# Performance work log

Hardware: AMD Instinct MI355X
Metric: run time of the kernel (lower is better)

Reference implementation:

```python
import jax, jax.numpy as jnp
import numpy as np

K_EFF = 8           # top-k factors selected per token (init k, < num_factors)
TEMPERATURE = 1.0   # forward() default


def setup_inputs() -> dict:
    key = jax.random.key(0)
    k1, k2 = jax.random.split(key)
    N, M = 131072, 512
    logits = jax.random.normal(k1, (N, M), dtype=jnp.float32)
    beta_qb = jax.random.normal(k2, (M,), dtype=jnp.float32)
    return {"logits": logits, "beta_qb": beta_qb}


def reference(logits, beta_qb):
    """Quantile-balanced sparse gating forward (eval path).

    Top-k selection on debiased logits (logits - beta_qb); probabilities are a
    softmax over the selected RAW logits, scattered back to a dense [N, M] map.
    """
    N, M = logits.shape
    # debiased scores only steer the hard top-k selection
    scores_adj = logits - beta_qb[None, :]                 # [N, M]
    _, topk_idx = jax.lax.top_k(scores_adj, K_EFF)         # [N, k]
    # gather raw logits at selected factors, softmax over the k slots
    selected = jnp.take_along_axis(logits, topk_idx, axis=-1)   # [N, k]
    selected_probs = jax.nn.softmax(selected / TEMPERATURE, axis=-1)
    # scatter sparse probabilities back into dense [N, M]
    rows = jnp.arange(N)[:, None]                          # [N, 1]
    probs = jnp.zeros_like(logits).at[rows, topk_idx].set(selected_probs)
    return probs
```

## Files before the change

### kernel.cpp

```cpp
#include <hip/hip_runtime.h>


constexpr int M_DIM = 512;

template<int CTRL, int RMASK>
__device__ __forceinline__ unsigned wmax_step(unsigned v) {
    int y = __builtin_amdgcn_update_dpp((int)v, (int)v, CTRL, RMASK, 0xF, false);
    unsigned u = (unsigned)y;
    return u > v ? u : v;
}

__device__ __forceinline__ unsigned wave_max_u32(unsigned v) {
    v = wmax_step<0x111, 0xF>(v);
    v = wmax_step<0x112, 0xF>(v);
    v = wmax_step<0x114, 0xF>(v);
    v = wmax_step<0x118, 0xF>(v);
    v = wmax_step<0x142, 0xA>(v);
    v = wmax_step<0x143, 0xC>(v);
    return (unsigned)__builtin_amdgcn_readlane((int)v, 63);
}

template<int S>
__device__ __forceinline__ void round_step(unsigned key[8], const float raw[8],
                                           unsigned M[8], unsigned win,
                                           float& rawt, int lane, bool rereduce) {
    unsigned long long mm = __ballot(key[S] == win);
    int wl = (int)__builtin_ctzll(mm);
    rawt = __int_as_float(__builtin_amdgcn_readlane(__float_as_int(raw[S]), wl));
    if (lane == wl) key[S] = 0u;
    if (rereduce) M[S] = wave_max_u32(key[S]);
}

__global__ __launch_bounds__(256, 8)
void qb_gating_kernel(const float* __restrict__ logits,
                      const float* __restrict__ beta,
                      float* __restrict__ out,
                      int nrows)
{
    const int lane   = threadIdx.x & 63;
    const int gwave  = (int)((blockIdx.x * blockDim.x + threadIdx.x) >> 6);
    const int nwaves = (int)((gridDim.x * blockDim.x) >> 6);

    const int base0 = 4 * lane;
    const int base1 = 256 + 4 * lane;

    const float4 b0 = *(const float4*)(beta + base0);
    const float4 b1 = *(const float4*)(beta + base1);
    const float bb[8] = {b0.x, b0.y, b0.z, b0.w, b1.x, b1.y, b1.z, b1.w};

    for (int row = gwave; row < nrows; row += nwaves) {
        const float* rp = logits + (size_t)row * M_DIM;
        const float4 r0 = *(const float4*)(rp + base0);
        const float4 r1 = *(const float4*)(rp + base1);
        float raw[8] = {r0.x, r0.y, r0.z, r0.w, r1.x, r1.y, r1.z, r1.w};

        unsigned key[8];
#pragma unroll
        for (int s = 0; s < 8; ++s) {
            const float a = raw[s] - bb[s];
            const int u = __float_as_int(a);
            key[s] = (unsigned)(u ^ ((u >> 31) | 0x80000000));
        }

        unsigned M[8];
#pragma unroll
        for (int s = 0; s < 8; ++s) M[s] = wave_max_u32(key[s]);

        float sraw[8];
#pragma unroll
        for (int t = 0; t < 8; ++t) {
            unsigned best = M[0]; int ss = 0;
#pragma unroll
            for (int s = 1; s < 8; ++s) {
                if (M[s] > best) { best = M[s]; ss = s; }
            }
#define ROUND_CASE(S) case S: round_step<S>(key, raw, M, best, sraw[t], lane, t < 7); break;
            switch (ss) {
                ROUND_CASE(0) ROUND_CASE(1) ROUND_CASE(2) ROUND_CASE(3)
                ROUND_CASE(4) ROUND_CASE(5) ROUND_CASE(6) ROUND_CASE(7)
            }
#undef ROUND_CASE
        }

        float m = sraw[0];
#pragma unroll
        for (int t = 1; t < 8; ++t) m = fmaxf(m, sraw[t]);
        float sum = 0.f;
#pragma unroll
        for (int t = 0; t < 8; ++t) sum += __expf(sraw[t] - m);
        const float inv = __builtin_amdgcn_rcpf(sum);

        float o[8];
#pragma unroll
        for (int s = 0; s < 8; ++s)
            o[s] = (key[s] == 0u) ? __expf(raw[s] - m) * inv : 0.f;

        float* op = out + (size_t)row * M_DIM;
        *(float4*)(op + base0) = make_float4(o[0], o[1], o[2], o[3]);
        *(float4*)(op + base1) = make_float4(o[4], o[5], o[6], o[7]);
    }
}

extern "C" void kernel_launch(void* const* d_in, const int* in_sizes, int n_in,
                              void* d_out, int out_size, void* d_ws, size_t ws_size,
                              hipStream_t stream)
{
    const float* logits = (const float*)d_in[0];
    const float* beta   = (const float*)d_in[1];
    float*       out    = (float*)d_out;

    const int nrows = in_sizes[0] / M_DIM;

    qb_gating_kernel<<<4096, 256, 0, stream>>>(logits, beta, out, nrows);
}
```

Before: 449.9 us.

## Replace iterative argmax top-k with ballot-based binary search on threshold

Instead of eight rounds of wave max reductions to extract top-k, the kernel binary-searches the 32-bit sortable key space for a threshold where exactly 8 elements are at or above it, counting with ballots and popcounts. Ties at the boundary are broken by lane prefix counts. The softmax now uses exp of raw logits without max subtraction and a DPP wave sum. This risks overflow for large logits and can take up to 32 search iterations of 8 ballots each per row.

```diff
diff --git a/kernel.cpp b/kernel.cpp
--- a/kernel.cpp
+++ b/kernel.cpp
@@ -4,31 +4,19 @@
 constexpr int M_DIM = 512;
 
 template<int CTRL, int RMASK>
-__device__ __forceinline__ unsigned wmax_step(unsigned v) {
-    int y = __builtin_amdgcn_update_dpp((int)v, (int)v, CTRL, RMASK, 0xF, false);
-    unsigned u = (unsigned)y;
-    return u > v ? u : v;
+__device__ __forceinline__ float wsum_step(float v) {
+    int y = __builtin_amdgcn_update_dpp(0, __float_as_int(v), CTRL, RMASK, 0xF, true);
+    return v + __int_as_float(y);
 }
 
-__device__ __forceinline__ unsigned wave_max_u32(unsigned v) {
-    v = wmax_step<0x111, 0xF>(v);
-    v = wmax_step<0x112, 0xF>(v);
-    v = wmax_step<0x114, 0xF>(v);
-    v = wmax_step<0x118, 0xF>(v);
-    v = wmax_step<0x142, 0xA>(v);
-    v = wmax_step<0x143, 0xC>(v);
-    return (unsigned)__builtin_amdgcn_readlane((int)v, 63);
-}
-
-template<int S>
-__device__ __forceinline__ void round_step(unsigned key[8], const float raw[8],
-                                           unsigned M[8], unsigned win,
-                                           float& rawt, int lane, bool rereduce) {
-    unsigned long long mm = __ballot(key[S] == win);
-    int wl = (int)__builtin_ctzll(mm);
-    rawt = __int_as_float(__builtin_amdgcn_readlane(__float_as_int(raw[S]), wl));
-    if (lane == wl) key[S] = 0u;
-    if (rereduce) M[S] = wave_max_u32(key[S]);
+__device__ __forceinline__ float wave_sum_f32(float v) {
+    v = wsum_step<0x111, 0xF>(v);
+    v = wsum_step<0x112, 0xF>(v);
+    v = wsum_step<0x114, 0xF>(v);
+    v = wsum_step<0x118, 0xF>(v);
+    v = wsum_step<0x142, 0xA>(v);
+    v = wsum_step<0x143, 0xC>(v);
+    return __int_as_float(__builtin_amdgcn_readlane(__float_as_int(v), 63));
 }
 
 __global__ __launch_bounds__(256, 8)
@@ -52,52 +40,69 @@
         const float* rp = logits + (size_t)row * M_DIM;
         const float4 r0 = *(const float4*)(rp + base0);
         const float4 r1 = *(const float4*)(rp + base1);
-        float raw[8] = {r0.x, r0.y, r0.z, r0.w, r1.x, r1.y, r1.z, r1.w};
+        const float raw[8] = {r0.x, r0.y, r0.z, r0.w, r1.x, r1.y, r1.z, r1.w};
 
         unsigned key[8];
 #pragma unroll
         for (int s = 0; s < 8; ++s) {
-            const float a = raw[s] - bb[s];
-            const int u = __float_as_int(a);
+            const int u = __float_as_int(raw[s] - bb[s]);
             key[s] = (unsigned)(u ^ ((u >> 31) | 0x80000000));
         }
 
-        unsigned M[8];
+        unsigned lo = 0u, hi = 0xFFFFFFFFu, T = 0u;
+        bool found = false;
+        while (hi - lo > 1u) {
+            const unsigned mid = lo + ((hi - lo) >> 1);
+            int c = 0;
 #pragma unroll
-        for (int s = 0; s < 8; ++s) M[s] = wave_max_u32(key[s]);
-
-        float sraw[8];
-#pragma unroll
-        for (int t = 0; t < 8; ++t) {
-            unsigned best = M[0]; int ss = 0;
-#pragma unroll
-            for (int s = 1; s < 8; ++s) {
-                if (M[s] > best) { best = M[s]; ss = s; }
+            for (int s = 0; s < 8; ++s)
+                c += __popcll(__ballot(key[s] >= mid));
+            if (c >= 8) {
+                lo = mid;
+                if (c == 8) { T = mid; found = true; break; }
+            } else {
+                hi = mid;
             }
-#define ROUND_CASE(S) case S: round_step<S>(key, raw, M, best, sraw[t], lane, t < 7); break;
-            switch (ss) {
-                ROUND_CASE(0) ROUND_CASE(1) ROUND_CASE(2) ROUND_CASE(3)
-                ROUND_CASE(4) ROUND_CASE(5) ROUND_CASE(6) ROUND_CASE(7)
-            }
-#undef ROUND_CASE
         }
 
-        float m = sraw[0];
+        bool sel[8];
+        if (found) {
 #pragma unroll
-        for (int t = 1; t < 8; ++t) m = fmaxf(m, sraw[t]);
-        float sum = 0.f;
+            for (int s = 0; s < 8; ++s) sel[s] = key[s] >= T;
+        } else {
+            int need = 8;
 #pragma unroll
-        for (int t = 0; t < 8; ++t) sum += __expf(sraw[t] - m);
-        const float inv = __builtin_amdgcn_rcpf(sum);
+            for (int s = 0; s < 8; ++s) {
+                sel[s] = key[s] > lo;
+                need -= __popcll(__ballot(sel[s]));
+            }
+#pragma unroll
+            for (int s = 0; s < 8; ++s) {
+                const unsigned long long m = __ballot(key[s] == lo);
+                int take = (int)__popcll(m);
+                take = take < need ? take : need;
+                const int pfx = (int)__builtin_amdgcn_mbcnt_hi(
+                    (unsigned)(m >> 32),
+                    __builtin_amdgcn_mbcnt_lo((unsigned)m, 0u));
+                if ((key[s] == lo) && (pfx < take)) sel[s] = true;
+                need -= take;
+            }
+        }
 
-        float o[8];
+        float e[8];
+        float psum = 0.f;
 #pragma unroll
-        for (int s = 0; s < 8; ++s)
-            o[s] = (key[s] == 0u) ? __expf(raw[s] - m) * inv : 0.f;
+        for (int s = 0; s < 8; ++s) {
+            const float ex = __expf(raw[s]);
+            e[s] = sel[s] ? ex : 0.f;
+            psum += e[s];
+        }
+        const float tot = wave_sum_f32(psum);
+        const float inv = __builtin_amdgcn_rcpf(tot);
 
         float* op = out + (size_t)row * M_DIM;
-        *(float4*)(op + base0) = make_float4(o[0], o[1], o[2], o[3]);
-        *(float4*)(op + base1) = make_float4(o[4], o[5], o[6], o[7]);
+        *(float4*)(op + base0) = make_float4(e[0]*inv, e[1]*inv, e[2]*inv, e[3]*inv);
+        *(float4*)(op + base1) = make_float4(e[4]*inv, e[5]*inv, e[6]*inv, e[7]*inv);
     }
 }
 
```

New measurement: 443.7 us. About the same (-1.4%).
